# Kernel optimization log

Hardware: AMD Instinct MI355X
Metric: run time of the kernel (lower is better)

## Reference

```python
import jax, jax.numpy as jnp
import numpy as np

MUL = 16          # multiplicity of every irrep block
N = 131072        # number of nodes

# orthonormal traceless-symmetric 3x3 basis, divided by sqrt(5).
_s = 1.0 / np.sqrt(2.0)
_M = np.zeros((5, 3, 3), dtype=np.float32)
_M[0, 0, 1] = _M[0, 1, 0] = _s
_M[1, 0, 2] = _M[1, 2, 0] = _s
_M[2, 1, 2] = _M[2, 2, 1] = _s
_M[3, 0, 0] = _s; _M[3, 1, 1] = -_s
_M[4] = np.diag([-1.0, -1.0, 2.0]).astype(np.float32) / np.sqrt(6.0)
C112 = jnp.asarray(np.transpose(_M, (1, 2, 0)) / np.sqrt(5.0))  # (3,3,5)

# e3nn TensorProduct normalization: irrep_normalization='component'
# (alpha = 2l_out+1), path_normalization='element' (divide by sum of
# mul_u*mul_v over paths into the same output irrep). 0e output receives
# two paths -> 2*MUL^2; 1o and 2e each receive one path -> MUL^2.
A000 = float(np.sqrt(1.0 / (2.0 * MUL * MUL)))                    # 0e x 0e -> 0e (w3j = 1)
A110 = float(np.sqrt(1.0 / (2.0 * MUL * MUL)) / np.sqrt(3.0))     # 1o x 1o -> 0e (w3j = d_ij/sqrt(3))
A101 = float(np.sqrt(3.0 / (MUL * MUL)) / np.sqrt(3.0))           # 1o x 0e -> 1o (w3j = d_ik/sqrt(3))
A112 = float(np.sqrt(5.0 / (MUL * MUL)))                          # 1o x 1o -> 2e


def setup_inputs() -> dict:
    key = jax.random.key(0)
    ks = jax.random.split(key, 6)
    f = lambda k, s: jax.random.normal(k, s, dtype=jnp.float32)
    return {
        "node_feats": f(ks[0], (N, 4 * MUL)),
        "node_messages": f(ks[1], (N, 4 * MUL)),
        "w000": f(ks[2], (MUL, MUL, MUL)),
        "w101": f(ks[3], (MUL, MUL, MUL)),
        "w110": f(ks[4], (MUL, MUL, MUL)),
        "w112": f(ks[5], (MUL, MUL, MUL)),
    }


def _tensor_square(x, w000, w101, w110, w112):
    """e3nn o3.TensorSquare('16x0e+16x1o', '16x0e+16x1o+16x2e') with 'uvw' weighted paths."""
    n = x.shape[0]
    x0 = x[:, :MUL]                          # (n, u)     l=0 block
    x1 = x[:, MUL:].reshape(n, MUL, 3)       # (n, u, i)  l=1 block (mul-major)

    # --- 0e output ---
    out0 = A000 * jnp.einsum('uvw,nu,nv->nw', w000, x0, x0)
    out0 = out0 + A110 * jnp.einsum('uvw,nui,nvi->nw', w110, x1, x1)

    # --- 1o output ---
    out1 = A101 * jnp.einsum('uvw,nuk,nv->nwk', w101, x1, x0)

    # --- 2e output (staged to keep intermediates small) ---
    t1 = jnp.einsum('nvj,ijk->nvik', x1, C112)        # (n, v, i, 5)
    t = jnp.einsum('nui,nvik->nuvk', x1, t1)          # (n, u, v, 5)
    out2 = A112 * jnp.einsum('uvw,nuvk->nwk', w112, t)

    return jnp.concatenate(
        [out0, out1.reshape(n, 3 * MUL), out2.reshape(n, 5 * MUL)], axis=1
    )  # (n, 144)


def reference(node_feats, node_messages, w000, w101, w110, w112):
    # SimpleNodeBlock: sum all nodewise tensors, then tensor square.
    return _tensor_square(node_feats + node_messages, w000, w101, w110, w112)
```

## Files before the change

### kernel.cpp

```cpp
#include <hip/hip_runtime.h>

#define MUL 16
#define NTILE 30
#define NCHUNK 6

typedef __bf16 bf16x8 __attribute__((ext_vector_type(8)));
typedef float  f32x2  __attribute__((ext_vector_type(2)));
typedef float  f32x4  __attribute__((ext_vector_type(4)));

__device__ __forceinline__ void group_uvs(int g, int& u, int& vs) {
    if (g < 16) { u = g >> 1; vs = u + ((g & 1) << 3); }
    else        { u = g - 8;  vs = u; }
}

__global__ void prep_weights(const float* __restrict__ w000,
                             const float* __restrict__ w101,
                             const float* __restrict__ w110,
                             const float* __restrict__ w112,
                             __bf16* __restrict__ wt) {
    const int gid = blockIdx.x * 256 + threadIdx.x;
    if (gid >= NTILE * 64) return;
    const int T = gid >> 6, lane = gid & 63;
    const int q = lane >> 4, w = lane & 15;

    const float A000   = 0.044194173824159216f;
    const float A110   = 0.025515518153991442f;
    const float A101   = 0.0625f;
    const float A112C1 = 0.044194173824159216f;

    bf16x8 frag = {};
    if (T < 12) {
        const int c = T >> 1, h = T & 1;
        int u, vs; group_uvs(4 * c + q, u, vs);
#pragma unroll
        for (int i = 0; i < 4; ++i) {
            const int v = vs + 4 * h + i;
            if (v < 16) {
                const int uvw = (u * MUL + v) * MUL + w;
                const int vuw = (v * MUL + u) * MUL + w;
                float f000, f110;
                if (u == v) { f000 = A000 * w000[uvw]; f110 = A110 * w110[uvw]; }
                else        { f000 = A000 * (w000[uvw] + w000[vuw]);
                              f110 = A110 * (w110[uvw] + w110[vuw]); }
                frag[2 * i]     = (__bf16)f000;
                frag[2 * i + 1] = (__bf16)f110;
            }
        }
    } else if (T < 24) {
        const int c = (T - 12) >> 1, h = (T - 12) & 1;
        int u, vs; group_uvs(4 * c + q, u, vs);
#pragma unroll
        for (int i = 0; i < 4; ++i) {
            const int v = vs + 4 * h + i;
            if (v < 16) {
                const int uvw = (u * MUL + v) * MUL + w;
                const int vuw = (v * MUL + u) * MUL + w;
                frag[2 * i]     = (__bf16)(A101 * w101[uvw]);
                frag[2 * i + 1] = (__bf16)((u == v) ? 0.f : A101 * w101[vuw]);
            }
        }
    } else {
        const int c = T - 24;
        int u, vs; group_uvs(4 * c + q, u, vs);
#pragma unroll
        for (int e = 0; e < 8; ++e) {
            const int v = vs + e;
            if (v < 16) {
                const int uvw = (u * MUL + v) * MUL + w;
                const int vuw = (v * MUL + u) * MUL + w;
                const float f112 = (u == v) ? A112C1 * w112[uvw]
                                            : A112C1 * (w112[uvw] + w112[vuw]);
                frag[e] = (__bf16)f112;
            }
        }
    }
    ((bf16x8*)wt)[T * 64 + lane] = frag;
}

#define SQ3f  1.7320508075688772f
#define ISQ3f 0.5773502691896258f

template<int J>
__device__ __forceinline__ void do_pair(int vs, const float* __restrict__ xrow,
        const float4 xu,
        bf16x8& fS, bf16x8& f0, bf16x8& f1, bf16x8& f2,
        bf16x8& t0, bf16x8& t1, bf16x8& t2, bf16x8& t3, bf16x8& t4) {
    int v = vs + J;
    v = v < 15 ? v : 15;
    const float4 xv = *(const float4*)(xrow + 4 * v);

    const f32x2 U01 = {xu.x, xu.y};
    const f32x2 U23 = {xu.z, xu.w};
    const f32x2 U10 = {xu.y, xu.x};
    const f32x2 V01 = {xv.x, xv.y};
    const f32x2 V23 = {xv.z, xv.w};
    const f32x2 V10 = {xv.y, xv.x};
    const f32x2 V32 = {xv.w, xv.z};

    const f32x2 P1 = U01 * V01;
    const f32x2 P2 = U23 * V23;
    const f32x2 P3 = U01 * V23;
    const f32x2 P4 = U23 * V01;
    const f32x2 P5 = U01 * V32;
    const f32x2 P6 = U23 * V10;
    const f32x2 P7 = U23 * V32;
    const f32x2 P8 = U10 * V01;

    const float o00 = P1[1], o11 = P2[0], o22 = P2[1];
    const float s1 = (o00 + o11) + o22;

    constexpr int s2 = (J & 3) * 2;
    fS[s2]     = (__bf16)P1[0];  fS[s2 + 1] = (__bf16)s1;
    f0[s2]     = (__bf16)P8[0];  f0[s2 + 1] = (__bf16)P8[1];
    f1[s2]     = (__bf16)P4[0];  f1[s2 + 1] = (__bf16)P3[0];
    f2[s2]     = (__bf16)P6[1];  f2[s2 + 1] = (__bf16)P5[0];
    t0[J] = (__bf16)(P5[1] + P6[0]);
    t1[J] = (__bf16)(P3[1] + P4[1]);
    t2[J] = (__bf16)(P7[0] + P7[1]);
    t3[J] = (__bf16)(o00 - o11);
    t4[J] = (__bf16)(SQ3f * o22 - ISQ3f * s1);
}

__launch_bounds__(256, 3)
__global__ void tsq_kernel(const float* __restrict__ feats,
                           const float* __restrict__ msgs,
                           const __bf16* __restrict__ wtiles,
                           float* __restrict__ out) {
    __shared__ __align__(16) float smem[4][2304];

    const int tid  = threadIdx.x;
    const int lane = tid & 63;
    const int wid  = tid >> 6;
    float* sw = smem[wid];

    const long long waveNode = (long long)blockIdx.x * 64 + wid * 16;

    {
        const int v = lane & 15, g = lane >> 4;
#pragma unroll
        for (int k = 0; k < 4; ++k) {
            const int nd = g * 4 + k;
            const float* fp = feats + (waveNode + nd) * 64;
            const float* mp = msgs  + (waveNode + nd) * 64;
            float4 qd;
            qd.x = fp[v]          + mp[v];
            qd.y = fp[16 + 3 * v] + mp[16 + 3 * v];
            qd.z = fp[17 + 3 * v] + mp[17 + 3 * v];
            qd.w = fp[18 + 3 * v] + mp[18 + 3 * v];
            *(float4*)&sw[nd * 68 + 4 * v] = qd;
        }
    }
    __syncthreads();

    const int m = lane & 15, q = lane >> 4;
    const float* xrow = sw + m * 68;
    const bf16x8* wb = (const bf16x8*)wtiles;

    f32x4 accS  = {0.f, 0.f, 0.f, 0.f};
    f32x4 accP0 = {0.f, 0.f, 0.f, 0.f};
    f32x4 accP1 = {0.f, 0.f, 0.f, 0.f};
    f32x4 accP2 = {0.f, 0.f, 0.f, 0.f};
    f32x4 accT0 = {0.f, 0.f, 0.f, 0.f};
    f32x4 accT1 = {0.f, 0.f, 0.f, 0.f};
    f32x4 accT2 = {0.f, 0.f, 0.f, 0.f};
    f32x4 accT3 = {0.f, 0.f, 0.f, 0.f};
    f32x4 accT4 = {0.f, 0.f, 0.f, 0.f};

#pragma unroll
    for (int c = 0; c < NCHUNK; ++c) {
        const bf16x8 bS0 = wb[(2 * c) * 64 + lane];
        const bf16x8 bS1 = wb[(2 * c + 1) * 64 + lane];
        const bf16x8 bP0 = wb[(12 + 2 * c) * 64 + lane];
        const bf16x8 bP1 = wb[(13 + 2 * c) * 64 + lane];
        const bf16x8 bT  = wb[(24 + c) * 64 + lane];

        int u, vs;
        if (c < 4) { u = 2 * c + (q >> 1); vs = u + ((q & 1) << 3); }
        else       { u = 4 * c - 8 + q;    vs = u; }
        const float4 xu = *(const float4*)(xrow + 4 * u);

        bf16x8 t0 = {}, t1 = {}, t2 = {}, t3 = {}, t4 = {};
        {
            bf16x8 fS, f0, f1, f2;
            do_pair<0>(vs, xrow, xu, fS, f0, f1, f2, t0, t1, t2, t3, t4);
            do_pair<1>(vs, xrow, xu, fS, f0, f1, f2, t0, t1, t2, t3, t4);
            do_pair<2>(vs, xrow, xu, fS, f0, f1, f2, t0, t1, t2, t3, t4);
            do_pair<3>(vs, xrow, xu, fS, f0, f1, f2, t0, t1, t2, t3, t4);
            accS  = __builtin_amdgcn_mfma_f32_16x16x32_bf16(fS, bS0, accS,  0, 0, 0);
            accP0 = __builtin_amdgcn_mfma_f32_16x16x32_bf16(f0, bP0, accP0, 0, 0, 0);
            accP1 = __builtin_amdgcn_mfma_f32_16x16x32_bf16(f1, bP0, accP1, 0, 0, 0);
            accP2 = __builtin_amdgcn_mfma_f32_16x16x32_bf16(f2, bP0, accP2, 0, 0, 0);
        }
        {
            bf16x8 fS, f0, f1, f2;
            do_pair<4>(vs, xrow, xu, fS, f0, f1, f2, t0, t1, t2, t3, t4);
            do_pair<5>(vs, xrow, xu, fS, f0, f1, f2, t0, t1, t2, t3, t4);
            do_pair<6>(vs, xrow, xu, fS, f0, f1, f2, t0, t1, t2, t3, t4);
            do_pair<7>(vs, xrow, xu, fS, f0, f1, f2, t0, t1, t2, t3, t4);
            accS  = __builtin_amdgcn_mfma_f32_16x16x32_bf16(fS, bS1, accS,  0, 0, 0);
            accP0 = __builtin_amdgcn_mfma_f32_16x16x32_bf16(f0, bP1, accP0, 0, 0, 0);
            accP1 = __builtin_amdgcn_mfma_f32_16x16x32_bf16(f1, bP1, accP1, 0, 0, 0);
            accP2 = __builtin_amdgcn_mfma_f32_16x16x32_bf16(f2, bP1, accP2, 0, 0, 0);
        }
        accT0 = __builtin_amdgcn_mfma_f32_16x16x32_bf16(t0, bT, accT0, 0, 0, 0);
        accT1 = __builtin_amdgcn_mfma_f32_16x16x32_bf16(t1, bT, accT1, 0, 0, 0);
        accT2 = __builtin_amdgcn_mfma_f32_16x16x32_bf16(t2, bT, accT2, 0, 0, 0);
        accT3 = __builtin_amdgcn_mfma_f32_16x16x32_bf16(t3, bT, accT3, 0, 0, 0);
        accT4 = __builtin_amdgcn_mfma_f32_16x16x32_bf16(t4, bT, accT4, 0, 0, 0);
    }

    __syncthreads();

#pragma unroll
    for (int r = 0; r < 4; ++r) {
        float* eb = sw + (q * 4 + r) * 144;
        eb[m]              = accS[r];
        eb[16 + 3 * m + 0] = accP0[r];
        eb[16 + 3 * m + 1] = accP1[r];
        eb[16 + 3 * m + 2] = accP2[r];
        eb[64 + 5 * m + 0] = accT0[r];
        eb[64 + 5 * m + 1] = accT1[r];
        eb[64 + 5 * m + 2] = accT2[r];
        eb[64 + 5 * m + 3] = accT3[r];
        eb[64 + 5 * m + 4] = accT4[r];
    }
    __syncthreads();

    {
        const float4* ep4 = (const float4*)sw;
        float4* ob4 = (float4*)(out + waveNode * 144);
#pragma unroll
        for (int l = 0; l < 9; ++l)
            ob4[l * 64 + lane] = ep4[l * 64 + lane];
    }
}

extern "C" void kernel_launch(void* const* d_in, const int* in_sizes, int n_in,
                              void* d_out, int out_size, void* d_ws, size_t ws_size,
                              hipStream_t stream) {
    const float* feats = (const float*)d_in[0];
    const float* msgs  = (const float*)d_in[1];
    const float* w000  = (const float*)d_in[2];
    const float* w101  = (const float*)d_in[3];
    const float* w110  = (const float*)d_in[4];
    const float* w112  = (const float*)d_in[5];
    __bf16* wt = (__bf16*)d_ws;
    float* out = (float*)d_out;

    const int n = in_sizes[0] / (4 * MUL);

    prep_weights<<<(NTILE * 64 + 255) / 256, 256, 0, stream>>>(w000, w101, w110, w112, wt);
    tsq_kernel<<<n / 64, 256, 0, stream>>>(feats, msgs, wt, out);
}
```

Measured before the change: 157.3 us.

## Process two node tiles per wave, prefetching second tile during first compute

Each block now handles 128 nodes, and each wave processes two 16-node tiles back to back. The global loads for the second tile are issued midway through the first tile's MFMA chunks and held in registers, so memory latency overlaps with compute. Block-wide __syncthreads are replaced by a per-wave s_waitcnt lgkmcnt(0) plus a scheduling barrier, since each wave only uses its own LDS slice. The cost is higher register pressure from the prefetched data, and fewer blocks in the grid.

```diff
diff --git a/kernel.cpp b/kernel.cpp
--- a/kernel.cpp
+++ b/kernel.cpp
@@ -80,6 +80,11 @@
 #define SQ3f  1.7320508075688772f
 #define ISQ3f 0.5773502691896258f
 
+#define WAIT_LDS() do {                                     \
+        asm volatile("s_waitcnt lgkmcnt(0)" ::: "memory");  \
+        __builtin_amdgcn_sched_barrier(0);                  \
+    } while (0)
+
 template<int J>
 __device__ __forceinline__ void do_pair(int vs, const float* __restrict__ xrow,
         const float4 xu,
@@ -121,6 +126,71 @@
     t4[J] = (__bf16)(SQ3f * o22 - ISQ3f * s1);
 }
 
+#define DO_CHUNK(cc)                                                          \
+    {                                                                         \
+        constexpr int c = (cc);                                               \
+        const bf16x8 bS0 = wb[(2 * c) * 64 + lane];                           \
+        const bf16x8 bS1 = wb[(2 * c + 1) * 64 + lane];                       \
+        const bf16x8 bP0 = wb[(12 + 2 * c) * 64 + lane];                      \
+        const bf16x8 bP1 = wb[(13 + 2 * c) * 64 + lane];                      \
+        const bf16x8 bT  = wb[(24 + c) * 64 + lane];                          \
+        int u, vs;                                                            \
+        if (c < 4) { u = 2 * c + (q >> 1); vs = u + ((q & 1) << 3); }         \
+        else       { u = 4 * c - 8 + q;    vs = u; }                          \
+        const float4 xu = *(const float4*)(xrow + 4 * u);                     \
+        bf16x8 t0 = {}, t1 = {}, t2 = {}, t3 = {}, t4 = {};                   \
+        {                                                                     \
+            bf16x8 fS, f0, f1, f2;                                            \
+            do_pair<0>(vs, xrow, xu, fS, f0, f1, f2, t0, t1, t2, t3, t4);     \
+            do_pair<1>(vs, xrow, xu, fS, f0, f1, f2, t0, t1, t2, t3, t4);     \
+            do_pair<2>(vs, xrow, xu, fS, f0, f1, f2, t0, t1, t2, t3, t4);     \
+            do_pair<3>(vs, xrow, xu, fS, f0, f1, f2, t0, t1, t2, t3, t4);     \
+            accS  = __builtin_amdgcn_mfma_f32_16x16x32_bf16(fS, bS0, accS,  0, 0, 0); \
+            accP0 = __builtin_amdgcn_mfma_f32_16x16x32_bf16(f0, bP0, accP0, 0, 0, 0); \
+            accP1 = __builtin_amdgcn_mfma_f32_16x16x32_bf16(f1, bP0, accP1, 0, 0, 0); \
+            accP2 = __builtin_amdgcn_mfma_f32_16x16x32_bf16(f2, bP0, accP2, 0, 0, 0); \
+        }                                                                     \
+        {                                                                     \
+            bf16x8 fS, f0, f1, f2;                                            \
+            do_pair<4>(vs, xrow, xu, fS, f0, f1, f2, t0, t1, t2, t3, t4);     \
+            do_pair<5>(vs, xrow, xu, fS, f0, f1, f2, t0, t1, t2, t3, t4);     \
+            do_pair<6>(vs, xrow, xu, fS, f0, f1, f2, t0, t1, t2, t3, t4);     \
+            do_pair<7>(vs, xrow, xu, fS, f0, f1, f2, t0, t1, t2, t3, t4);     \
+            accS  = __builtin_amdgcn_mfma_f32_16x16x32_bf16(fS, bS1, accS,  0, 0, 0); \
+            accP0 = __builtin_amdgcn_mfma_f32_16x16x32_bf16(f0, bP1, accP0, 0, 0, 0); \
+            accP1 = __builtin_amdgcn_mfma_f32_16x16x32_bf16(f1, bP1, accP1, 0, 0, 0); \
+            accP2 = __builtin_amdgcn_mfma_f32_16x16x32_bf16(f2, bP1, accP2, 0, 0, 0); \
+        }                                                                     \
+        accT0 = __builtin_amdgcn_mfma_f32_16x16x32_bf16(t0, bT, accT0, 0, 0, 0); \
+        accT1 = __builtin_amdgcn_mfma_f32_16x16x32_bf16(t1, bT, accT1, 0, 0, 0); \
+        accT2 = __builtin_amdgcn_mfma_f32_16x16x32_bf16(t2, bT, accT2, 0, 0, 0); \
+        accT3 = __builtin_amdgcn_mfma_f32_16x16x32_bf16(t3, bT, accT3, 0, 0, 0); \
+        accT4 = __builtin_amdgcn_mfma_f32_16x16x32_bf16(t4, bT, accT4, 0, 0, 0); \
+    }
+
+#define EPILOGUE(nodeBase)                                                    \
+    {                                                                         \
+        _Pragma("unroll")                                                     \
+        for (int r = 0; r < 4; ++r) {                                         \
+            float* eb = sw + (q * 4 + r) * 144;                               \
+            eb[m]              = accS[r];                                     \
+            eb[16 + 3 * m + 0] = accP0[r];                                    \
+            eb[16 + 3 * m + 1] = accP1[r];                                    \
+            eb[16 + 3 * m + 2] = accP2[r];                                    \
+            eb[64 + 5 * m + 0] = accT0[r];                                    \
+            eb[64 + 5 * m + 1] = accT1[r];                                    \
+            eb[64 + 5 * m + 2] = accT2[r];                                    \
+            eb[64 + 5 * m + 3] = accT3[r];                                    \
+            eb[64 + 5 * m + 4] = accT4[r];                                    \
+        }                                                                     \
+        WAIT_LDS();                                                           \
+        const float4* ep4 = (const float4*)sw;                                \
+        float4* ob4 = (float4*)(out + (nodeBase) * 144);                      \
+        _Pragma("unroll")                                                     \
+        for (int l = 0; l < 9; ++l)                                           \
+            ob4[l * 64 + lane] = ep4[l * 64 + lane];                          \
+    }
+
 __launch_bounds__(256, 3)
 __global__ void tsq_kernel(const float* __restrict__ feats,
                            const float* __restrict__ msgs,
@@ -133,28 +203,26 @@
     const int wid  = tid >> 6;
     float* sw = smem[wid];
 
-    const long long waveNode = (long long)blockIdx.x * 64 + wid * 16;
-
-    {
-        const int v = lane & 15, g = lane >> 4;
-#pragma unroll
-        for (int k = 0; k < 4; ++k) {
-            const int nd = g * 4 + k;
-            const float* fp = feats + (waveNode + nd) * 64;
-            const float* mp = msgs  + (waveNode + nd) * 64;
-            float4 qd;
-            qd.x = fp[v]          + mp[v];
-            qd.y = fp[16 + 3 * v] + mp[16 + 3 * v];
-            qd.z = fp[17 + 3 * v] + mp[17 + 3 * v];
-            qd.w = fp[18 + 3 * v] + mp[18 + 3 * v];
-            *(float4*)&sw[nd * 68 + 4 * v] = qd;
-        }
-    }
-    __syncthreads();
-
     const int m = lane & 15, q = lane >> 4;
     const float* xrow = sw + m * 68;
     const bf16x8* wb = (const bf16x8*)wtiles;
+
+    const long long nodeA = (long long)blockIdx.x * 128 + wid * 16;
+    const long long nodeB = nodeA + 64;
+
+#pragma unroll
+    for (int k = 0; k < 4; ++k) {
+        const int nd = q * 4 + k;
+        const float* fp = feats + (nodeA + nd) * 64;
+        const float* mp = msgs  + (nodeA + nd) * 64;
+        float4 qd;
+        qd.x = fp[m]          + mp[m];
+        qd.y = fp[16 + 3 * m] + mp[16 + 3 * m];
+        qd.z = fp[17 + 3 * m] + mp[17 + 3 * m];
+        qd.w = fp[18 + 3 * m] + mp[18 + 3 * m];
+        *(float4*)&sw[nd * 68 + 4 * m] = qd;
+    }
+    WAIT_LDS();
 
     f32x4 accS  = {0.f, 0.f, 0.f, 0.f};
     f32x4 accP0 = {0.f, 0.f, 0.f, 0.f};
@@ -166,73 +234,58 @@
     f32x4 accT3 = {0.f, 0.f, 0.f, 0.f};
     f32x4 accT4 = {0.f, 0.f, 0.f, 0.f};
 
-#pragma unroll
-    for (int c = 0; c < NCHUNK; ++c) {
-        const bf16x8 bS0 = wb[(2 * c) * 64 + lane];
-        const bf16x8 bS1 = wb[(2 * c + 1) * 64 + lane];
-        const bf16x8 bP0 = wb[(12 + 2 * c) * 64 + lane];
-        const bf16x8 bP1 = wb[(13 + 2 * c) * 64 + lane];
-        const bf16x8 bT  = wb[(24 + c) * 64 + lane];
-
-        int u, vs;
-        if (c < 4) { u = 2 * c + (q >> 1); vs = u + ((q & 1) << 3); }
-        else       { u = 4 * c - 8 + q;    vs = u; }
-        const float4 xu = *(const float4*)(xrow + 4 * u);
-
-        bf16x8 t0 = {}, t1 = {}, t2 = {}, t3 = {}, t4 = {};
-        {
-            bf16x8 fS, f0, f1, f2;
-            do_pair<0>(vs, xrow, xu, fS, f0, f1, f2, t0, t1, t2, t3, t4);
-            do_pair<1>(vs, xrow, xu, fS, f0, f1, f2, t0, t1, t2, t3, t4);
-            do_pair<2>(vs, xrow, xu, fS, f0, f1, f2, t0, t1, t2, t3, t4);
-            do_pair<3>(vs, xrow, xu, fS, f0, f1, f2, t0, t1, t2, t3, t4);
-            accS  = __builtin_amdgcn_mfma_f32_16x16x32_bf16(fS, bS0, accS,  0, 0, 0);
-            accP0 = __builtin_amdgcn_mfma_f32_16x16x32_bf16(f0, bP0, accP0, 0, 0, 0);
-            accP1 = __builtin_amdgcn_mfma_f32_16x16x32_bf16(f1, bP0, accP1, 0, 0, 0);
-            accP2 = __builtin_amdgcn_mfma_f32_16x16x32_bf16(f2, bP0, accP2, 0, 0, 0);
-        }
-        {
-            bf16x8 fS, f0, f1, f2;
-            do_pair<4>(vs, xrow, xu, fS, f0, f1, f2, t0, t1, t2, t3, t4);
-            do_pair<5>(vs, xrow, xu, fS, f0, f1, f2, t0, t1, t2, t3, t4);
-            do_pair<6>(vs, xrow, xu, fS, f0, f1, f2, t0, t1, t2, t3, t4);
-            do_pair<7>(vs, xrow, xu, fS, f0, f1, f2, t0, t1, t2, t3, t4);
-            accS  = __builtin_amdgcn_mfma_f32_16x16x32_bf16(fS, bS1, accS,  0, 0, 0);
-            accP0 = __builtin_amdgcn_mfma_f32_16x16x32_bf16(f0, bP1, accP0, 0, 0, 0);
-            accP1 = __builtin_amdgcn_mfma_f32_16x16x32_bf16(f1, bP1, accP1, 0, 0, 0);
-            accP2 = __builtin_amdgcn_mfma_f32_16x16x32_bf16(f2, bP1, accP2, 0, 0, 0);
-        }
-        accT0 = __builtin_amdgcn_mfma_f32_16x16x32_bf16(t0, bT, accT0, 0, 0, 0);
-        accT1 = __builtin_amdgcn_mfma_f32_16x16x32_bf16(t1, bT, accT1, 0, 0, 0);
-        accT2 = __builtin_amdgcn_mfma_f32_16x16x32_bf16(t2, bT, accT2, 0, 0, 0);
-        accT3 = __builtin_amdgcn_mfma_f32_16x16x32_bf16(t3, bT, accT3, 0, 0, 0);
-        accT4 = __builtin_amdgcn_mfma_f32_16x16x32_bf16(t4, bT, accT4, 0, 0, 0);
-    }
-
-    __syncthreads();
-
-#pragma unroll
-    for (int r = 0; r < 4; ++r) {
-        float* eb = sw + (q * 4 + r) * 144;
-        eb[m]              = accS[r];
-        eb[16 + 3 * m + 0] = accP0[r];
-        eb[16 + 3 * m + 1] = accP1[r];
-        eb[16 + 3 * m + 2] = accP2[r];
-        eb[64 + 5 * m + 0] = accT0[r];
-        eb[64 + 5 * m + 1] = accT1[r];
-        eb[64 + 5 * m + 2] = accT2[r];
-        eb[64 + 5 * m + 3] = accT3[r];
-        eb[64 + 5 * m + 4] = accT4[r];
-    }
-    __syncthreads();
-
-    {
-        const float4* ep4 = (const float4*)sw;
-        float4* ob4 = (float4*)(out + waveNode * 144);
-#pragma unroll
-        for (int l = 0; l < 9; ++l)
-            ob4[l * 64 + lane] = ep4[l * 64 + lane];
-    }
+    DO_CHUNK(0)
+    DO_CHUNK(1)
+    DO_CHUNK(2)
+
+    float4 fB[4], mB[4];
+#pragma unroll
+    for (int k = 0; k < 4; ++k) {
+        const int nd = q * 4 + k;
+        const float* fp = feats + (nodeB + nd) * 64;
+        const float* mp = msgs  + (nodeB + nd) * 64;
+        fB[k].x = fp[m];          mB[k].x = mp[m];
+        fB[k].y = fp[16 + 3 * m]; mB[k].y = mp[16 + 3 * m];
+        fB[k].z = fp[17 + 3 * m]; mB[k].z = mp[17 + 3 * m];
+        fB[k].w = fp[18 + 3 * m]; mB[k].w = mp[18 + 3 * m];
+    }
+
+    DO_CHUNK(3)
+    DO_CHUNK(4)
+    DO_CHUNK(5)
+
+    EPILOGUE(nodeA)
+
+#pragma unroll
+    for (int k = 0; k < 4; ++k) {
+        const int nd = q * 4 + k;
+        float4 qd;
+        qd.x = fB[k].x + mB[k].x;
+        qd.y = fB[k].y + mB[k].y;
+        qd.z = fB[k].z + mB[k].z;
+        qd.w = fB[k].w + mB[k].w;
+        *(float4*)&sw[nd * 68 + 4 * m] = qd;
+    }
+    WAIT_LDS();
+
+    accS  = (f32x4){0.f, 0.f, 0.f, 0.f};
+    accP0 = (f32x4){0.f, 0.f, 0.f, 0.f};
+    accP1 = (f32x4){0.f, 0.f, 0.f, 0.f};
+    accP2 = (f32x4){0.f, 0.f, 0.f, 0.f};
+    accT0 = (f32x4){0.f, 0.f, 0.f, 0.f};
+    accT1 = (f32x4){0.f, 0.f, 0.f, 0.f};
+    accT2 = (f32x4){0.f, 0.f, 0.f, 0.f};
+    accT3 = (f32x4){0.f, 0.f, 0.f, 0.f};
+    accT4 = (f32x4){0.f, 0.f, 0.f, 0.f};
+
+    DO_CHUNK(0)
+    DO_CHUNK(1)
+    DO_CHUNK(2)
+    DO_CHUNK(3)
+    DO_CHUNK(4)
+    DO_CHUNK(5)
+
+    EPILOGUE(nodeB)
 }
 
 extern "C" void kernel_launch(void* const* d_in, const int* in_sizes, int n_in,
@@ -250,5 +303,5 @@
     const int n = in_sizes[0] / (4 * MUL);
 
     prep_weights<<<(NTILE * 64 + 255) / 256, 256, 0, stream>>>(w000, w101, w110, w112, wt);
-    tsq_kernel<<<n / 64, 256, 0, stream>>>(feats, msgs, wt, out);
-}
+    tsq_kernel<<<n / 128, 256, 0, stream>>>(feats, msgs, wt, out);
+}
```

Measured after the change: 375.8 us. 139% more time.

## Rotate u/v pairing into registers, drop LDS staging of inputs

Applied to the files above, without the earlier changes.

Each lane now loads its node's full 64-float input row straight from global memory into registers, rotated by the lane group. Pairs are enumerated as a cyclic offset c=(v-u) mod 16, which gives 9 uniform chunks of MFMA work in place of 6 uneven chunks with clamped indices. The weight tiles are repacked to match, and block-wide barriers are swapped for a per-wave LDS wait. This removes the LDS round trip and per-pair shared loads, at the cost of many more registers (occupancy hint drops from 3 to 2), more redundant global reads per lane, and 9 tensor-term MFMAs where there were 6.

```diff
diff --git a/kernel.cpp b/kernel.cpp
--- a/kernel.cpp
+++ b/kernel.cpp
@@ -1,17 +1,11 @@
 #include <hip/hip_runtime.h>
 
 #define MUL 16
-#define NTILE 30
-#define NCHUNK 6
+#define NTILE 27
+#define NCHUNK 9
 
 typedef __bf16 bf16x8 __attribute__((ext_vector_type(8)));
-typedef float  f32x2  __attribute__((ext_vector_type(2)));
 typedef float  f32x4  __attribute__((ext_vector_type(4)));
-
-__device__ __forceinline__ void group_uvs(int g, int& u, int& vs) {
-    if (g < 16) { u = g >> 1; vs = u + ((g & 1) << 3); }
-    else        { u = g - 8;  vs = u; }
-}
 
 __global__ void prep_weights(const float* __restrict__ w000,
                              const float* __restrict__ w101,
@@ -22,57 +16,38 @@
     if (gid >= NTILE * 64) return;
     const int T = gid >> 6, lane = gid & 63;
     const int q = lane >> 4, w = lane & 15;
+    const int fam = T / 9;
+    const int c = T % 9;
 
     const float A000   = 0.044194173824159216f;
     const float A110   = 0.025515518153991442f;
     const float A101   = 0.0625f;
     const float A112C1 = 0.044194173824159216f;
 
+    const bool mid = (c >= 1 && c <= 7);
+
     bf16x8 frag = {};
-    if (T < 12) {
-        const int c = T >> 1, h = T & 1;
-        int u, vs; group_uvs(4 * c + q, u, vs);
-#pragma unroll
-        for (int i = 0; i < 4; ++i) {
-            const int v = vs + 4 * h + i;
-            if (v < 16) {
-                const int uvw = (u * MUL + v) * MUL + w;
-                const int vuw = (v * MUL + u) * MUL + w;
-                float f000, f110;
-                if (u == v) { f000 = A000 * w000[uvw]; f110 = A110 * w110[uvw]; }
-                else        { f000 = A000 * (w000[uvw] + w000[vuw]);
-                              f110 = A110 * (w110[uvw] + w110[vuw]); }
-                frag[2 * i]     = (__bf16)f000;
-                frag[2 * i + 1] = (__bf16)f110;
-            }
+#pragma unroll
+    for (int e = 0; e < 8; ++e) {
+        const int u = (4 * q + e) & 15;
+        const int v = (u + c) & 15;
+        const int p = e >> 2;
+        const int uvw = (u * MUL + v) * MUL + w;
+        const int vuw = (v * MUL + u) * MUL + w;
+        float val;
+        if (fam == 0) {
+            val = (p == 0)
+                ? A000 * (mid ? (w000[uvw] + w000[vuw]) : w000[uvw])
+                : A110 * (mid ? (w110[uvw] + w110[vuw]) : w110[uvw]);
+        } else if (fam == 1) {
+            val = (p == 0) ? A101 * w101[uvw]
+                           : (mid ? A101 * w101[vuw] : 0.f);
+        } else {
+            val = (p == 0)
+                ? A112C1 * (mid ? (w112[uvw] + w112[vuw]) : w112[uvw])
+                : 0.f;
         }
-    } else if (T < 24) {
-        const int c = (T - 12) >> 1, h = (T - 12) & 1;
-        int u, vs; group_uvs(4 * c + q, u, vs);
-#pragma unroll
-        for (int i = 0; i < 4; ++i) {
-            const int v = vs + 4 * h + i;
-            if (v < 16) {
-                const int uvw = (u * MUL + v) * MUL + w;
-                const int vuw = (v * MUL + u) * MUL + w;
-                frag[2 * i]     = (__bf16)(A101 * w101[uvw]);
-                frag[2 * i + 1] = (__bf16)((u == v) ? 0.f : A101 * w101[vuw]);
-            }
-        }
-    } else {
-        const int c = T - 24;
-        int u, vs; group_uvs(4 * c + q, u, vs);
-#pragma unroll
-        for (int e = 0; e < 8; ++e) {
-            const int v = vs + e;
-            if (v < 16) {
-                const int uvw = (u * MUL + v) * MUL + w;
-                const int vuw = (v * MUL + u) * MUL + w;
-                const float f112 = (u == v) ? A112C1 * w112[uvw]
-                                            : A112C1 * (w112[uvw] + w112[vuw]);
-                frag[e] = (__bf16)f112;
-            }
-        }
+        frag[e] = (__bf16)val;
     }
     ((bf16x8*)wt)[T * 64 + lane] = frag;
 }
@@ -80,48 +55,66 @@
 #define SQ3f  1.7320508075688772f
 #define ISQ3f 0.5773502691896258f
 
-template<int J>
-__device__ __forceinline__ void do_pair(int vs, const float* __restrict__ xrow,
-        const float4 xu,
-        bf16x8& fS, bf16x8& f0, bf16x8& f1, bf16x8& f2,
-        bf16x8& t0, bf16x8& t1, bf16x8& t2, bf16x8& t3, bf16x8& t4) {
-    int v = vs + J;
-    v = v < 15 ? v : 15;
-    const float4 xv = *(const float4*)(xrow + 4 * v);
-
-    const f32x2 U01 = {xu.x, xu.y};
-    const f32x2 U23 = {xu.z, xu.w};
-    const f32x2 U10 = {xu.y, xu.x};
-    const f32x2 V01 = {xv.x, xv.y};
-    const f32x2 V23 = {xv.z, xv.w};
-    const f32x2 V10 = {xv.y, xv.x};
-    const f32x2 V32 = {xv.w, xv.z};
-
-    const f32x2 P1 = U01 * V01;
-    const f32x2 P2 = U23 * V23;
-    const f32x2 P3 = U01 * V23;
-    const f32x2 P4 = U23 * V01;
-    const f32x2 P5 = U01 * V32;
-    const f32x2 P6 = U23 * V10;
-    const f32x2 P7 = U23 * V32;
-    const f32x2 P8 = U10 * V01;
-
-    const float o00 = P1[1], o11 = P2[0], o22 = P2[1];
-    const float s1 = (o00 + o11) + o22;
-
-    constexpr int s2 = (J & 3) * 2;
-    fS[s2]     = (__bf16)P1[0];  fS[s2 + 1] = (__bf16)s1;
-    f0[s2]     = (__bf16)P8[0];  f0[s2 + 1] = (__bf16)P8[1];
-    f1[s2]     = (__bf16)P4[0];  f1[s2 + 1] = (__bf16)P3[0];
-    f2[s2]     = (__bf16)P6[1];  f2[s2 + 1] = (__bf16)P5[0];
-    t0[J] = (__bf16)(P5[1] + P6[0]);
-    t1[J] = (__bf16)(P3[1] + P4[1]);
-    t2[J] = (__bf16)(P7[0] + P7[1]);
-    t3[J] = (__bf16)(o00 - o11);
-    t4[J] = (__bf16)(SQ3f * o22 - ISQ3f * s1);
-}
-
-__launch_bounds__(256, 3)
+#define WAIT_LDS() do {                                     \
+        asm volatile("s_waitcnt lgkmcnt(0)" ::: "memory");  \
+        __builtin_amdgcn_sched_barrier(0);                  \
+    } while (0)
+
+template<int C>
+__device__ __forceinline__ void do_chunk(
+        const float (&x0)[16], const float (&x1)[48],
+        const bf16x8* __restrict__ wb, int lane,
+        f32x4& accS, f32x4& accP0, f32x4& accP1, f32x4& accP2,
+        f32x4& accT0, f32x4& accT1, f32x4& accT2, f32x4& accT3, f32x4& accT4)
+{
+    const bf16x8 bS = wb[C * 64 + lane];
+    const bf16x8 bP = wb[(9 + C) * 64 + lane];
+    const bf16x8 bT = wb[(18 + C) * 64 + lane];
+
+    bf16x8 fS, f0, f1, f2;
+    bf16x8 t0 = {}, t1 = {}, t2 = {}, t3 = {}, t4 = {};
+
+#pragma unroll
+    for (int j = 0; j < 4; ++j) {
+        const int vp = (j + C) & 15;
+        const float Ux = x0[j],  U0 = x1[3*j],  U1 = x1[3*j+1],  U2 = x1[3*j+2];
+        const float Vx = x0[vp], V0 = x1[3*vp], V1 = x1[3*vp+1], V2 = x1[3*vp+2];
+        fS[j] = (__bf16)(Ux * Vx);
+        f0[j] = (__bf16)(U0 * Vx);
+        f1[j] = (__bf16)(U1 * Vx);
+        f2[j] = (__bf16)(U2 * Vx);
+        const float o00 = U0*V0, o01 = U0*V1, o02 = U0*V2;
+        const float o10 = U1*V0, o11 = U1*V1, o12 = U1*V2;
+        const float o20 = U2*V0, o21 = U2*V1, o22 = U2*V2;
+        t0[j] = (__bf16)(o01 + o10);
+        t1[j] = (__bf16)(o02 + o20);
+        t2[j] = (__bf16)(o12 + o21);
+        t3[j] = (__bf16)(o00 - o11);
+        t4[j] = (__bf16)(SQ3f * o22 - ISQ3f * ((o00 + o11) + o22));
+    }
+#pragma unroll
+    for (int j = 4; j < 8; ++j) {
+        const int vp = (j + C) & 15;
+        const float Ux = x0[j],  U0 = x1[3*j],  U1 = x1[3*j+1],  U2 = x1[3*j+2];
+        const float Vx = x0[vp], V0 = x1[3*vp], V1 = x1[3*vp+1], V2 = x1[3*vp+2];
+        fS[j] = (__bf16)(U0*V0 + U1*V1 + U2*V2);
+        f0[j] = (__bf16)(V0 * Ux);
+        f1[j] = (__bf16)(V1 * Ux);
+        f2[j] = (__bf16)(V2 * Ux);
+    }
+
+    accS  = __builtin_amdgcn_mfma_f32_16x16x32_bf16(fS, bS, accS,  0, 0, 0);
+    accP0 = __builtin_amdgcn_mfma_f32_16x16x32_bf16(f0, bP, accP0, 0, 0, 0);
+    accP1 = __builtin_amdgcn_mfma_f32_16x16x32_bf16(f1, bP, accP1, 0, 0, 0);
+    accP2 = __builtin_amdgcn_mfma_f32_16x16x32_bf16(f2, bP, accP2, 0, 0, 0);
+    accT0 = __builtin_amdgcn_mfma_f32_16x16x32_bf16(t0, bT, accT0, 0, 0, 0);
+    accT1 = __builtin_amdgcn_mfma_f32_16x16x32_bf16(t1, bT, accT1, 0, 0, 0);
+    accT2 = __builtin_amdgcn_mfma_f32_16x16x32_bf16(t2, bT, accT2, 0, 0, 0);
+    accT3 = __builtin_amdgcn_mfma_f32_16x16x32_bf16(t3, bT, accT3, 0, 0, 0);
+    accT4 = __builtin_amdgcn_mfma_f32_16x16x32_bf16(t4, bT, accT4, 0, 0, 0);
+}
+
+__launch_bounds__(256, 2)
 __global__ void tsq_kernel(const float* __restrict__ feats,
                            const float* __restrict__ msgs,
                            const __bf16* __restrict__ wtiles,
@@ -133,28 +126,33 @@
     const int wid  = tid >> 6;
     float* sw = smem[wid];
 
+    const int m = lane & 15, q = lane >> 4;
     const long long waveNode = (long long)blockIdx.x * 64 + wid * 16;
-
-    {
-        const int v = lane & 15, g = lane >> 4;
-#pragma unroll
-        for (int k = 0; k < 4; ++k) {
-            const int nd = g * 4 + k;
-            const float* fp = feats + (waveNode + nd) * 64;
-            const float* mp = msgs  + (waveNode + nd) * 64;
-            float4 qd;
-            qd.x = fp[v]          + mp[v];
-            qd.y = fp[16 + 3 * v] + mp[16 + 3 * v];
-            qd.z = fp[17 + 3 * v] + mp[17 + 3 * v];
-            qd.w = fp[18 + 3 * v] + mp[18 + 3 * v];
-            *(float4*)&sw[nd * 68 + 4 * v] = qd;
-        }
-    }
-    __syncthreads();
-
-    const int m = lane & 15, q = lane >> 4;
-    const float* xrow = sw + m * 68;
-    const bf16x8* wb = (const bf16x8*)wtiles;
+    const float* fp = feats + (waveNode + m) * 64;
+    const float* mp = msgs  + (waveNode + m) * 64;
+
+    float x0[16], x1[48];
+#pragma unroll
+    for (int k = 0; k < 4; ++k) {
+        const int off = (4 * q + 4 * k) & 15;
+        const float4 a = *(const float4*)(fp + off);
+        const float4 b = *(const float4*)(mp + off);
+        x0[4*k+0] = a.x + b.x;
+        x0[4*k+1] = a.y + b.y;
+        x0[4*k+2] = a.z + b.z;
+        x0[4*k+3] = a.w + b.w;
+    }
+#pragma unroll
+    for (int r = 0; r < 12; ++r) {
+        int off = 12 * q + 4 * r;
+        off = (off >= 48) ? off - 48 : off;
+        const float4 a = *(const float4*)(fp + 16 + off);
+        const float4 b = *(const float4*)(mp + 16 + off);
+        x1[4*r+0] = a.x + b.x;
+        x1[4*r+1] = a.y + b.y;
+        x1[4*r+2] = a.z + b.z;
+        x1[4*r+3] = a.w + b.w;
+    }
 
     f32x4 accS  = {0.f, 0.f, 0.f, 0.f};
     f32x4 accP0 = {0.f, 0.f, 0.f, 0.f};
@@ -166,50 +164,16 @@
     f32x4 accT3 = {0.f, 0.f, 0.f, 0.f};
     f32x4 accT4 = {0.f, 0.f, 0.f, 0.f};
 
-#pragma unroll
-    for (int c = 0; c < NCHUNK; ++c) {
-        const bf16x8 bS0 = wb[(2 * c) * 64 + lane];
-        const bf16x8 bS1 = wb[(2 * c + 1) * 64 + lane];
-        const bf16x8 bP0 = wb[(12 + 2 * c) * 64 + lane];
-        const bf16x8 bP1 = wb[(13 + 2 * c) * 64 + lane];
-        const bf16x8 bT  = wb[(24 + c) * 64 + lane];
-
-        int u, vs;
-        if (c < 4) { u = 2 * c + (q >> 1); vs = u + ((q & 1) << 3); }
-        else       { u = 4 * c - 8 + q;    vs = u; }
-        const float4 xu = *(const float4*)(xrow + 4 * u);
-
-        bf16x8 t0 = {}, t1 = {}, t2 = {}, t3 = {}, t4 = {};
-        {
-            bf16x8 fS, f0, f1, f2;
-            do_pair<0>(vs, xrow, xu, fS, f0, f1, f2, t0, t1, t2, t3, t4);
-            do_pair<1>(vs, xrow, xu, fS, f0, f1, f2, t0, t1, t2, t3, t4);
-            do_pair<2>(vs, xrow, xu, fS, f0, f1, f2, t0, t1, t2, t3, t4);
-            do_pair<3>(vs, xrow, xu, fS, f0, f1, f2, t0, t1, t2, t3, t4);
-            accS  = __builtin_amdgcn_mfma_f32_16x16x32_bf16(fS, bS0, accS,  0, 0, 0);
-            accP0 = __builtin_amdgcn_mfma_f32_16x16x32_bf16(f0, bP0, accP0, 0, 0, 0);
-            accP1 = __builtin_amdgcn_mfma_f32_16x16x32_bf16(f1, bP0, accP1, 0, 0, 0);
-            accP2 = __builtin_amdgcn_mfma_f32_16x16x32_bf16(f2, bP0, accP2, 0, 0, 0);
-        }
-        {
-            bf16x8 fS, f0, f1, f2;
-            do_pair<4>(vs, xrow, xu, fS, f0, f1, f2, t0, t1, t2, t3, t4);
-            do_pair<5>(vs, xrow, xu, fS, f0, f1, f2, t0, t1, t2, t3, t4);
-            do_pair<6>(vs, xrow, xu, fS, f0, f1, f2, t0, t1, t2, t3, t4);
-            do_pair<7>(vs, xrow, xu, fS, f0, f1, f2, t0, t1, t2, t3, t4);
-            accS  = __builtin_amdgcn_mfma_f32_16x16x32_bf16(fS, bS1, accS,  0, 0, 0);
-            accP0 = __builtin_amdgcn_mfma_f32_16x16x32_bf16(f0, bP1, accP0, 0, 0, 0);
-            accP1 = __builtin_amdgcn_mfma_f32_16x16x32_bf16(f1, bP1, accP1, 0, 0, 0);
-            accP2 = __builtin_amdgcn_mfma_f32_16x16x32_bf16(f2, bP1, accP2, 0, 0, 0);
-        }
-        accT0 = __builtin_amdgcn_mfma_f32_16x16x32_bf16(t0, bT, accT0, 0, 0, 0);
-        accT1 = __builtin_amdgcn_mfma_f32_16x16x32_bf16(t1, bT, accT1, 0, 0, 0);
-        accT2 = __builtin_amdgcn_mfma_f32_16x16x32_bf16(t2, bT, accT2, 0, 0, 0);
-        accT3 = __builtin_amdgcn_mfma_f32_16x16x32_bf16(t3, bT, accT3, 0, 0, 0);
-        accT4 = __builtin_amdgcn_mfma_f32_16x16x32_bf16(t4, bT, accT4, 0, 0, 0);
-    }
-
-    __syncthreads();
+    const bf16x8* wb = (const bf16x8*)wtiles;
+    do_chunk<0>(x0, x1, wb, lane, accS, accP0, accP1, accP2, accT0, accT1, accT2, accT3, accT4);
+    do_chunk<1>(x0, x1, wb, lane, accS, accP0, accP1, accP2, accT0, accT1, accT2, accT3, accT4);
+    do_chunk<2>(x0, x1, wb, lane, accS, accP0, accP1, accP2, accT0, accT1, accT2, accT3, accT4);
+    do_chunk<3>(x0, x1, wb, lane, accS, accP0, accP1, accP2, accT0, accT1, accT2, accT3, accT4);
+    do_chunk<4>(x0, x1, wb, lane, accS, accP0, accP1, accP2, accT0, accT1, accT2, accT3, accT4);
+    do_chunk<5>(x0, x1, wb, lane, accS, accP0, accP1, accP2, accT0, accT1, accT2, accT3, accT4);
+    do_chunk<6>(x0, x1, wb, lane, accS, accP0, accP1, accP2, accT0, accT1, accT2, accT3, accT4);
+    do_chunk<7>(x0, x1, wb, lane, accS, accP0, accP1, accP2, accT0, accT1, accT2, accT3, accT4);
+    do_chunk<8>(x0, x1, wb, lane, accS, accP0, accP1, accP2, accT0, accT1, accT2, accT3, accT4);
 
 #pragma unroll
     for (int r = 0; r < 4; ++r) {
@@ -224,7 +188,7 @@
         eb[64 + 5 * m + 3] = accT3[r];
         eb[64 + 5 * m + 4] = accT4[r];
     }
-    __syncthreads();
+    WAIT_LDS();
 
     {
         const float4* ep4 = (const float4*)sw;
```

Measured after the change: 169.1 us. 1.07x slower.
